# Performance work log

Hardware: AMD Instinct MI355X
Metric: run time of the kernel (lower is better)

The kernel has to match this reference:

```python
import jax, jax.numpy as jnp
import numpy as np

L = 64          # chain length
D = 16          # bond dimension
S = 2           # local (spin) dimension
N = 131072      # batch of spin configurations


def setup_inputs() -> dict:
    key = jax.random.key(0)
    k1, k2, k3, k4 = jax.random.split(key, 4)
    scale = 1.0 / np.sqrt(D * S)  # matches init_tensors normal_(0, 1/sqrt(D*S))
    left = jax.random.normal(k1, (1, D, S), dtype=jnp.float32) * scale
    bulk = jax.random.normal(k2, (D, D, S), dtype=jnp.float32) * scale
    right = jax.random.normal(k3, (D, 1, S), dtype=jnp.float32) * scale
    x = jax.random.randint(k4, (N, L), 0, S)
    return {"x": x, "left": left, "bulk": bulk, "right": right}


def reference(x, left, bulk, right):
    # x: (N, L) int spins; amplitude(x) -> (N,)
    n, l = x.shape
    # left (1,D,S): gather left matrix per sample -> (N, D) (row vector, left bond is 1)
    leftT = left[0].T                      # (S, D)
    m0 = leftT[x[:, 0]]                    # (N, D)
    bulkT = jnp.transpose(bulk, (2, 0, 1))  # (S, D, D)
    xs = x[:, 1:l - 1].T                   # (L-2, N) bulk-site spins

    def step(m, s):
        # m: (N, D), bulkT[s]: (N, D, D) -> batched vec-mat product
        return jnp.einsum('nd,nde->ne', m, bulkT[s]), None

    m, _ = jax.lax.scan(step, m0, xs)      # (N, D)
    rightT = jnp.transpose(right, (2, 0, 1))[:, :, 0]  # (S, D)
    a = jnp.einsum('nd,nd->n', m, rightT[x[:, l - 1]])  # (N,)
    return a
```

## Files before the change

kernel.cpp:

```cpp
#include <hip/hip_runtime.h>

#define OFF_V    0u
#define OFF_W    262144u
#define OFF_P    524288u
#define OFF_VA   1048576u
#define OFF_WB   1050624u
#define OFF_PAV  1052672u
#define OFF_PAW  1085440u
#define OFF_PC0  1118208u
#define OFF_PC1  1150976u

__device__ __forceinline__ void rmul16(float* v, const float* B) {
  float nv[16];
#pragma unroll
  for (int e = 0; e < 16; ++e) {
    float a = 0.f;
#pragma unroll
    for (int d = 0; d < 16; ++d) a = fmaf(v[d], B[d * 16 + e], a);
    nv[e] = a;
  }
#pragma unroll
  for (int e = 0; e < 16; ++e) v[e] = nv[e];
}

__device__ __forceinline__ void lmul16(float* v, const float* B) {
  float nv[16];
#pragma unroll
  for (int d = 0; d < 16; ++d) {
    float a = 0.f;
#pragma unroll
    for (int e = 0; e < 16; ++e) a = fmaf(B[d * 16 + e], v[e], a);
    nv[d] = a;
  }
#pragma unroll
  for (int d = 0; d < 16; ++d) v[d] = nv[d];
}

__global__ __launch_bounds__(256) void build_a(const float* __restrict__ left,
                                               const float* __restrict__ bulk,
                                               const float* __restrict__ right,
                                               float* __restrict__ ws) {
  __shared__ float Bs[2][256];
  __shared__ float Ls[2][16];
  __shared__ float Rs[2][16];
  int tid = threadIdx.x;
  for (int i = tid; i < 576; i += 256) {
    if (i < 512) Bs[i & 1][i >> 1] = bulk[i];
    else if (i < 544) { int j = i - 512; Ls[j & 1][j >> 1] = left[j]; }
    else              { int j = i - 544; Rs[j & 1][j >> 1] = right[j]; }
  }
  __syncthreads();

  unsigned gid = blockIdx.x * 256 + tid;
  float v[16];
  if (gid < 128) {
    unsigned i = gid;
#pragma unroll
    for (int d = 0; d < 16; ++d) v[d] = Ls[i & 1][d];
    for (int t = 1; t <= 6; ++t) rmul16(v, Bs[(i >> t) & 1]);
#pragma unroll
    for (int d = 0; d < 16; ++d) ws[OFF_VA + i * 16 + d] = v[d];
  } else if (gid < 256) {
    unsigned i = gid - 128;
#pragma unroll
    for (int d = 0; d < 16; ++d) v[d] = Rs[(i >> 6) & 1][d];
    for (int p = 5; p >= 0; --p) lmul16(v, Bs[(i >> p) & 1]);
#pragma unroll
    for (int d = 0; d < 16; ++d) ws[OFF_WB + i * 16 + d] = v[d];
  } else if (gid < 2304) {
    unsigned it = gid - 256, i = it >> 4, col = it & 15;
#pragma unroll
    for (int d = 0; d < 16; ++d) v[d] = Bs[(i >> 6) & 1][d * 16 + col];
    for (int p = 5; p >= 0; --p) lmul16(v, Bs[(i >> p) & 1]);
#pragma unroll
    for (int d = 0; d < 16; ++d) ws[OFF_PAV + i * 256 + d * 16 + col] = v[d];
  } else if (gid < 4352) {
    unsigned it = gid - 2304, i = it >> 4, col = it & 15;
#pragma unroll
    for (int d = 0; d < 16; ++d) v[d] = Bs[(i >> 6) & 1][d * 16 + col];
    for (int p = 5; p >= 0; --p) lmul16(v, Bs[(i >> p) & 1]);
#pragma unroll
    for (int d = 0; d < 16; ++d) ws[OFF_PAW + i * 256 + d * 16 + col] = v[d];
  } else {
    unsigned it = gid - 4352, c = it / 768, r = it - c * 768;
    if (r < 512) {
      unsigned i = r >> 4, col = r & 15;
#pragma unroll
      for (int d = 0; d < 16; ++d) v[d] = Bs[(i >> 4) & 1][d * 16 + col];
      for (int p = 3; p >= 0; --p) lmul16(v, Bs[(i >> p) & 1]);
#pragma unroll
      for (int d = 0; d < 16; ++d) ws[OFF_PC0 + c * 8192 + i * 256 + d * 16 + col] = v[d];
    } else {
      unsigned r2 = r - 512, i = r2 >> 4, col = r2 & 15;
#pragma unroll
      for (int d = 0; d < 16; ++d) v[d] = Bs[(i >> 3) & 1][d * 16 + col];
      for (int p = 2; p >= 0; --p) lmul16(v, Bs[(i >> p) & 1]);
#pragma unroll
      for (int d = 0; d < 16; ++d) ws[OFF_PC1 + c * 4096 + i * 256 + d * 16 + col] = v[d];
    }
  }
}

__global__ __launch_bounds__(256) void build_b(float* __restrict__ ws) {
  unsigned gid = blockIdx.x * 256 + threadIdx.x;
  if (gid < 262144u) {
    unsigned i = gid >> 4, e = gid & 15;
    const float* va = ws + OFF_VA + (i & 127) * 16;
    const float* pm = ws + OFF_PAV + (i >> 7) * 256;
    float a = 0.f;
#pragma unroll
    for (int k = 0; k < 16; ++k) a = fmaf(va[k], pm[k * 16 + e], a);
    ws[OFF_V + (size_t)i * 16 + e] = a;
  } else if (gid < 524288u) {
    unsigned g = gid - 262144u, i = g >> 4, d = g & 15;
    const float* wb = ws + OFF_WB + (i >> 7) * 16;
    const float* pm = ws + OFF_PAW + (i & 127) * 256 + d * 16;
    float a = 0.f;
#pragma unroll
    for (int k = 0; k < 16; ++k) a = fmaf(pm[k], wb[k], a);
    ws[OFF_W + (size_t)i * 16 + d] = a;
  } else {
    unsigned g = gid - 524288u;
    unsigned c = g >> 17, rem = g & 131071u;
    unsigned idx = rem >> 8, d = (rem >> 4) & 15, e = rem & 15;
    const float* p0 = ws + OFF_PC0 + c * 8192 + (idx & 31) * 256 + d * 16;
    const float* p1 = ws + OFF_PC1 + c * 4096 + (idx >> 5) * 256 + e;
    float a = 0.f;
#pragma unroll
    for (int k = 0; k < 16; ++k) a = fmaf(p0[k], p1[k * 16], a);
    ws[OFF_P + ((size_t)c << 17) + (size_t)idx * 256 + d * 16 + e] = a;
  }
}

__global__ __launch_bounds__(256, 4) void mps_main(const int* __restrict__ x,
                                                   const float* __restrict__ ws,
                                                   float* __restrict__ out) {
  __shared__ float sm[4][4][16];
  const int tid = threadIdx.x;
  const int lane = tid & 63;
  const int wave = tid >> 6;
  const int grp = lane >> 4;
  const int e = lane & 15;
  const unsigned seqw = blockIdx.x * 16u + wave * 4u;
  const int* __restrict__ xp = x + (size_t)seqw * 64;

  int v0 = xp[lane];
  int v1 = xp[64 + lane];
  int v2 = xp[128 + lane];
  int v3 = xp[192 + lane];
  unsigned long long b0 = __ballot(v0 & 1);
  unsigned long long b1 = __ballot(v1 & 1);
  unsigned long long b2 = __ballot(v2 & 1);
  unsigned long long b3 = __ballot(v3 & 1);
  unsigned long long bits = (grp & 2) ? ((grp & 1) ? b3 : b2)
                                      : ((grp & 1) ? b1 : b0);

  const unsigned i0 = (unsigned)(bits & 0x3FFFull);
  const unsigned iw = (unsigned)(bits >> 50);
  unsigned idx0 = (unsigned)((bits >> 14) & 511ull);
  unsigned idx1 = (unsigned)((bits >> 23) & 511ull);
  unsigned idx2 = (unsigned)((bits >> 32) & 511ull);
  unsigned idx3 = (unsigned)((bits >> 41) & 511ull);

  float mv = ws[OFF_V + (size_t)i0 * 16 + e];
  float w  = ws[OFF_W + (size_t)iw * 16 + e];

  const float* __restrict__ P0 = ws + OFF_P;
  float p[4][16];
  {
    const float* pb = P0 + (size_t)idx0 * 256 + e;
#pragma unroll
    for (int d = 0; d < 16; ++d) p[0][d] = pb[d * 16];
  }
  {
    const float* pb = P0 + (1u << 17) + (size_t)idx1 * 256 + e;
#pragma unroll
    for (int d = 0; d < 16; ++d) p[1][d] = pb[d * 16];
  }
  {
    const float* pb = P0 + (2u << 17) + (size_t)idx2 * 256 + e;
#pragma unroll
    for (int d = 0; d < 16; ++d) p[2][d] = pb[d * 16];
  }
  {
    const float* pb = P0 + (3u << 17) + (size_t)idx3 * 256 + e;
#pragma unroll
    for (int d = 0; d < 16; ++d) p[3][d] = pb[d * 16];
  }

#pragma unroll
  for (int ch = 0; ch < 4; ++ch) {
    sm[wave][grp][e] = mv;
    asm volatile("" ::: "memory");
    float4 M0 = *(const float4*)&sm[wave][grp][0];
    float4 M1 = *(const float4*)&sm[wave][grp][4];
    float4 M2 = *(const float4*)&sm[wave][grp][8];
    float4 M3 = *(const float4*)&sm[wave][grp][12];
    asm volatile("" ::: "memory");
    float a0 = M0.x * p[ch][0];
    float a1 = M0.y * p[ch][1];
    float a2 = M0.z * p[ch][2];
    float a3 = M0.w * p[ch][3];
    a0 = fmaf(M1.x, p[ch][4], a0);
    a1 = fmaf(M1.y, p[ch][5], a1);
    a2 = fmaf(M1.z, p[ch][6], a2);
    a3 = fmaf(M1.w, p[ch][7], a3);
    a0 = fmaf(M2.x, p[ch][8], a0);
    a1 = fmaf(M2.y, p[ch][9], a1);
    a2 = fmaf(M2.z, p[ch][10], a2);
    a3 = fmaf(M2.w, p[ch][11], a3);
    a0 = fmaf(M3.x, p[ch][12], a0);
    a1 = fmaf(M3.y, p[ch][13], a1);
    a2 = fmaf(M3.z, p[ch][14], a2);
    a3 = fmaf(M3.w, p[ch][15], a3);
    mv = (a0 + a1) + (a2 + a3);
  }

  float part = mv * w;
  part += __shfl_xor(part, 1, 64);
  part += __shfl_xor(part, 2, 64);
  part += __shfl_xor(part, 4, 64);
  part += __shfl_xor(part, 8, 64);
  if (e == 0) out[seqw + grp] = part;
}

extern "C" void kernel_launch(void* const* d_in, const int* in_sizes, int n_in,
                              void* d_out, int out_size, void* d_ws, size_t ws_size,
                              hipStream_t stream) {
  const int* x = (const int*)d_in[0];
  const float* left = (const float*)d_in[1];
  const float* bulk = (const float*)d_in[2];
  const float* right = (const float*)d_in[3];
  float* out = (float*)d_out;
  float* ws = (float*)d_ws;

  int nseq = in_sizes[0] / 64;

  build_a<<<29, 256, 0, stream>>>(left, bulk, right, ws);
  build_b<<<4096, 256, 0, stream>>>(ws);
  mps_main<<<nseq / 16, 256, 0, stream>>>(x, ws, out);
}
```

Before: 119.9 us.

## Pack spin bits in build_a blocks so mps_main reads one 64-bit word

Extra blocks appended to the build_a launch read the 32 MB int spin array and ballot-pack each 64-site configuration into a 64-bit word stored in the workspace. mps_main then loads one packed word per sequence instead of reading and balloting the raw spins itself. The aim is to overlap the spin read with table construction and shrink the main kernel's memory traffic. The full input is still read once, and the packed array adds a write and read through the workspace.

Measured after the change: 120.9 us. About the same (+0.8%).

```diff
diff --git a/kernel.cpp b/kernel.cpp
--- a/kernel.cpp
+++ b/kernel.cpp
@@ -9,6 +9,7 @@
 #define OFF_PAW  1085440u
 #define OFF_PC0  1118208u
 #define OFF_PC1  1150976u
+#define OFF_PACK 1167360u
 
 __device__ __forceinline__ void rmul16(float* v, const float* B) {
   float nv[16];
@@ -39,11 +40,35 @@
 __global__ __launch_bounds__(256) void build_a(const float* __restrict__ left,
                                                const float* __restrict__ bulk,
                                                const float* __restrict__ right,
+                                               const int* __restrict__ x,
                                                float* __restrict__ ws) {
+  int tid = threadIdx.x;
+
+  if (blockIdx.x >= 29) {
+    int lane = tid & 63;
+    int wave = tid >> 6;
+    unsigned pb = blockIdx.x - 29;
+    unsigned seqbase = pb * 256u + wave * 64u;
+    const int* __restrict__ xp = x + (size_t)seqbase * 64;
+    unsigned long long word = 0ull;
+#pragma unroll
+    for (int rb = 0; rb < 8; ++rb) {
+      int vals[8];
+#pragma unroll
+      for (int j = 0; j < 8; ++j) vals[j] = xp[(size_t)(rb * 8 + j) * 64 + lane];
+#pragma unroll
+      for (int j = 0; j < 8; ++j) {
+        unsigned long long mm = __ballot(vals[j] & 1);
+        if (lane == rb * 8 + j) word = mm;
+      }
+    }
+    reinterpret_cast<unsigned long long*>(ws + OFF_PACK)[seqbase + lane] = word;
+    return;
+  }
+
   __shared__ float Bs[2][256];
   __shared__ float Ls[2][16];
   __shared__ float Rs[2][16];
-  int tid = threadIdx.x;
   for (int i = tid; i < 576; i += 256) {
     if (i < 512) Bs[i & 1][i >> 1] = bulk[i];
     else if (i < 544) { int j = i - 512; Ls[j & 1][j >> 1] = left[j]; }
@@ -132,8 +157,7 @@
   }
 }
 
-__global__ __launch_bounds__(256, 4) void mps_main(const int* __restrict__ x,
-                                                   const float* __restrict__ ws,
+__global__ __launch_bounds__(256, 4) void mps_main(const float* __restrict__ ws,
                                                    float* __restrict__ out) {
   __shared__ float sm[4][4][16];
   const int tid = threadIdx.x;
@@ -142,18 +166,9 @@
   const int grp = lane >> 4;
   const int e = lane & 15;
   const unsigned seqw = blockIdx.x * 16u + wave * 4u;
-  const int* __restrict__ xp = x + (size_t)seqw * 64;
-
-  int v0 = xp[lane];
-  int v1 = xp[64 + lane];
-  int v2 = xp[128 + lane];
-  int v3 = xp[192 + lane];
-  unsigned long long b0 = __ballot(v0 & 1);
-  unsigned long long b1 = __ballot(v1 & 1);
-  unsigned long long b2 = __ballot(v2 & 1);
-  unsigned long long b3 = __ballot(v3 & 1);
-  unsigned long long bits = (grp & 2) ? ((grp & 1) ? b3 : b2)
-                                      : ((grp & 1) ? b1 : b0);
+
+  unsigned long long bits =
+      reinterpret_cast<const unsigned long long*>(ws + OFF_PACK)[seqw + grp];
 
   const unsigned i0 = (unsigned)(bits & 0x3FFFull);
   const unsigned iw = (unsigned)(bits >> 50);
@@ -236,7 +251,7 @@
 
   int nseq = in_sizes[0] / 64;
 
-  build_a<<<29, 256, 0, stream>>>(left, bulk, right, ws);
+  build_a<<<29 + nseq / 256, 256, 0, stream>>>(left, bulk, right, x, ws);
   build_b<<<4096, 256, 0, stream>>>(ws);
-  mps_main<<<nseq / 16, 256, 0, stream>>>(x, ws, out);
-}
+  mps_main<<<nseq / 16, 256, 0, stream>>>(ws, out);
+}
```

## Shrink precomputed product tables to one 8-bit and four 7-bit chunks

Applied to the files above, without the earlier changes.

The middle-chain product tables change from four 9-bit chunks (512 matrices each) to one 8-bit and four 7-bit chunks, built directly in build_a. This removes the 524k-thread table-combine pass in build_b and shrinks the table footprint so it fits better in cache. In exchange, the main kernel loads five 16x16 matrix columns and runs five vector-matrix steps per sequence instead of four, and build_a does longer serial chains per thread. The x input is now read with nontemporal loads.

Measured after the change: 132.7 us. 1.11x slower.

```diff
diff --git a/kernel.cpp b/kernel.cpp
--- a/kernel.cpp
+++ b/kernel.cpp
@@ -3,12 +3,10 @@
 #define OFF_V    0u
 #define OFF_W    262144u
 #define OFF_P    524288u
-#define OFF_VA   1048576u
-#define OFF_WB   1050624u
-#define OFF_PAV  1052672u
-#define OFF_PAW  1085440u
-#define OFF_PC0  1118208u
-#define OFF_PC1  1150976u
+#define OFF_VA   720896u
+#define OFF_WB   722944u
+#define OFF_PAV  724992u
+#define OFF_PAW  757760u
 
 __device__ __forceinline__ void rmul16(float* v, const float* B) {
   float nv[16];
@@ -82,21 +80,23 @@
 #pragma unroll
     for (int d = 0; d < 16; ++d) ws[OFF_PAW + i * 256 + d * 16 + col] = v[d];
   } else {
-    unsigned it = gid - 4352, c = it / 768, r = it - c * 768;
-    if (r < 512) {
-      unsigned i = r >> 4, col = r & 15;
-#pragma unroll
-      for (int d = 0; d < 16; ++d) v[d] = Bs[(i >> 4) & 1][d * 16 + col];
-      for (int p = 3; p >= 0; --p) lmul16(v, Bs[(i >> p) & 1]);
-#pragma unroll
-      for (int d = 0; d < 16; ++d) ws[OFF_PC0 + c * 8192 + i * 256 + d * 16 + col] = v[d];
+    unsigned it = gid - 4352, mi = it >> 4, col = it & 15;
+    if (mi < 256) {
+      unsigned i = mi;
+#pragma unroll
+      for (int d = 0; d < 16; ++d) v[d] = Bs[(i >> 7) & 1][d * 16 + col];
+      for (int p = 6; p >= 0; --p) lmul16(v, Bs[(i >> p) & 1]);
+#pragma unroll
+      for (int d = 0; d < 16; ++d) ws[OFF_P + i * 256 + d * 16 + col] = v[d];
     } else {
-      unsigned r2 = r - 512, i = r2 >> 4, col = r2 & 15;
-#pragma unroll
-      for (int d = 0; d < 16; ++d) v[d] = Bs[(i >> 3) & 1][d * 16 + col];
-      for (int p = 2; p >= 0; --p) lmul16(v, Bs[(i >> p) & 1]);
-#pragma unroll
-      for (int d = 0; d < 16; ++d) ws[OFF_PC1 + c * 4096 + i * 256 + d * 16 + col] = v[d];
+      unsigned r = mi - 256;
+      unsigned c = r >> 7, i = r & 127;
+      unsigned base = 65536u + c * 32768u;
+#pragma unroll
+      for (int d = 0; d < 16; ++d) v[d] = Bs[(i >> 6) & 1][d * 16 + col];
+      for (int p = 5; p >= 0; --p) lmul16(v, Bs[(i >> p) & 1]);
+#pragma unroll
+      for (int d = 0; d < 16; ++d) ws[OFF_P + base + i * 256 + d * 16 + col] = v[d];
     }
   }
 }
@@ -111,7 +111,7 @@
 #pragma unroll
     for (int k = 0; k < 16; ++k) a = fmaf(va[k], pm[k * 16 + e], a);
     ws[OFF_V + (size_t)i * 16 + e] = a;
-  } else if (gid < 524288u) {
+  } else {
     unsigned g = gid - 262144u, i = g >> 4, d = g & 15;
     const float* wb = ws + OFF_WB + (i >> 7) * 16;
     const float* pm = ws + OFF_PAW + (i & 127) * 256 + d * 16;
@@ -119,16 +119,6 @@
 #pragma unroll
     for (int k = 0; k < 16; ++k) a = fmaf(pm[k], wb[k], a);
     ws[OFF_W + (size_t)i * 16 + d] = a;
-  } else {
-    unsigned g = gid - 524288u;
-    unsigned c = g >> 17, rem = g & 131071u;
-    unsigned idx = rem >> 8, d = (rem >> 4) & 15, e = rem & 15;
-    const float* p0 = ws + OFF_PC0 + c * 8192 + (idx & 31) * 256 + d * 16;
-    const float* p1 = ws + OFF_PC1 + c * 4096 + (idx >> 5) * 256 + e;
-    float a = 0.f;
-#pragma unroll
-    for (int k = 0; k < 16; ++k) a = fmaf(p0[k], p1[k * 16], a);
-    ws[OFF_P + ((size_t)c << 17) + (size_t)idx * 256 + d * 16 + e] = a;
   }
 }
 
@@ -144,10 +134,10 @@
   const unsigned seqw = blockIdx.x * 16u + wave * 4u;
   const int* __restrict__ xp = x + (size_t)seqw * 64;
 
-  int v0 = xp[lane];
-  int v1 = xp[64 + lane];
-  int v2 = xp[128 + lane];
-  int v3 = xp[192 + lane];
+  int v0 = __builtin_nontemporal_load(xp + lane);
+  int v1 = __builtin_nontemporal_load(xp + 64 + lane);
+  int v2 = __builtin_nontemporal_load(xp + 128 + lane);
+  int v3 = __builtin_nontemporal_load(xp + 192 + lane);
   unsigned long long b0 = __ballot(v0 & 1);
   unsigned long long b1 = __ballot(v1 & 1);
   unsigned long long b2 = __ballot(v2 & 1);
@@ -157,39 +147,45 @@
 
   const unsigned i0 = (unsigned)(bits & 0x3FFFull);
   const unsigned iw = (unsigned)(bits >> 50);
-  unsigned idx0 = (unsigned)((bits >> 14) & 511ull);
-  unsigned idx1 = (unsigned)((bits >> 23) & 511ull);
-  unsigned idx2 = (unsigned)((bits >> 32) & 511ull);
-  unsigned idx3 = (unsigned)((bits >> 41) & 511ull);
+  unsigned idx0 = (unsigned)((bits >> 14) & 255ull);
+  unsigned idx1 = (unsigned)((bits >> 22) & 127ull);
+  unsigned idx2 = (unsigned)((bits >> 29) & 127ull);
+  unsigned idx3 = (unsigned)((bits >> 36) & 127ull);
+  unsigned idx4 = (unsigned)((bits >> 43) & 127ull);
 
   float mv = ws[OFF_V + (size_t)i0 * 16 + e];
   float w  = ws[OFF_W + (size_t)iw * 16 + e];
 
   const float* __restrict__ P0 = ws + OFF_P;
-  float p[4][16];
+  float p[5][16];
   {
     const float* pb = P0 + (size_t)idx0 * 256 + e;
 #pragma unroll
     for (int d = 0; d < 16; ++d) p[0][d] = pb[d * 16];
   }
   {
-    const float* pb = P0 + (1u << 17) + (size_t)idx1 * 256 + e;
+    const float* pb = P0 + 65536u + (size_t)idx1 * 256 + e;
 #pragma unroll
     for (int d = 0; d < 16; ++d) p[1][d] = pb[d * 16];
   }
   {
-    const float* pb = P0 + (2u << 17) + (size_t)idx2 * 256 + e;
+    const float* pb = P0 + 98304u + (size_t)idx2 * 256 + e;
 #pragma unroll
     for (int d = 0; d < 16; ++d) p[2][d] = pb[d * 16];
   }
   {
-    const float* pb = P0 + (3u << 17) + (size_t)idx3 * 256 + e;
+    const float* pb = P0 + 131072u + (size_t)idx3 * 256 + e;
 #pragma unroll
     for (int d = 0; d < 16; ++d) p[3][d] = pb[d * 16];
   }
-
-#pragma unroll
-  for (int ch = 0; ch < 4; ++ch) {
+  {
+    const float* pb = P0 + 163840u + (size_t)idx4 * 256 + e;
+#pragma unroll
+    for (int d = 0; d < 16; ++d) p[4][d] = pb[d * 16];
+  }
+
+#pragma unroll
+  for (int ch = 0; ch < 5; ++ch) {
     sm[wave][grp][e] = mv;
     asm volatile("" ::: "memory");
     float4 M0 = *(const float4*)&sm[wave][grp][0];
@@ -236,7 +232,7 @@
 
   int nseq = in_sizes[0] / 64;
 
-  build_a<<<29, 256, 0, stream>>>(left, bulk, right, ws);
-  build_b<<<4096, 256, 0, stream>>>(ws);
+  build_a<<<65, 256, 0, stream>>>(left, bulk, right, ws);
+  build_b<<<2048, 256, 0, stream>>>(ws);
   mps_main<<<nseq / 16, 256, 0, stream>>>(x, ws, out);
 }
```
